# Kernel optimization log

Measured on AMD Instinct MI355X. Metric: run time of the kernel, lower is better.

Reference implementation:

```python
import jax, jax.numpy as jnp
import numpy as np
import math

NUM_HEADS = 8
RES_K = 9  # res_kernel_size


def setup_inputs() -> dict:
    key = jax.random.key(0)
    ks = jax.random.split(key, 6)
    N, C, h, w = 8, 256, 64, 64
    x = jax.random.normal(ks[0], (N, C, h, w), dtype=jnp.float32)
    w_qkv = jax.random.normal(ks[1], (3 * C, C), dtype=jnp.float32) * 0.02
    b_qkv = jax.random.normal(ks[2], (3 * C,), dtype=jnp.float32) * 0.02
    w_proj = jax.random.normal(ks[3], (C, C), dtype=jnp.float32) * 0.02
    b_proj = jax.random.normal(ks[4], (C,), dtype=jnp.float32) * 0.02
    w_dconv = jax.random.normal(ks[5], (NUM_HEADS, 1, RES_K, 1), dtype=jnp.float32) * 0.1
    return {"x": x, "w_qkv": w_qkv, "b_qkv": b_qkv,
            "w_proj": w_proj, "b_proj": b_proj, "w_dconv": w_dconv}


def _l2norm(t):
    # torch x / x.norm(dim=-1, keepdim=True): plain L2 norm, no eps
    return t / jnp.linalg.norm(t, axis=-1, keepdims=True)


def reference(x, w_qkv, b_qkv, w_proj, b_proj, w_dconv):
    N, C, h, w = x.shape
    H = NUM_HEADS
    D = C // H
    L = h * w
    xt = x.reshape(N, C, L).transpose(0, 2, 1)  # [N, L, C]
    qkv = xt @ w_qkv.T + b_qkv                   # [N, L, 3C]
    qkv = qkv.reshape(N, L, 3, H, D).transpose(2, 0, 3, 1, 4)  # [3, N, H, L, D]
    q, k, v = qkv[0], qkv[1], qkv[2]
    q = _l2norm(q)
    k = _l2norm(k)
    # depthwise conv over token dim: v as NCHW with C=H, H=L, W=D
    pad = RES_K // 2
    dconv_v = jax.lax.conv_general_dilated(
        v, w_dconv, window_strides=(1, 1), padding=[(pad, pad), (0, 0)],
        dimension_numbers=("NCHW", "OIHW", "NCHW"), feature_group_count=H)
    attn = jnp.einsum("nhld,nhle->nhde", k, v)   # [N, H, D, D]
    out = 0.5 * v + (1.0 / math.pi) * jnp.einsum("nhld,nhde->nhle", q, attn)
    out = _l2norm(out)
    out = out + dconv_v
    out = out.transpose(0, 2, 1, 3).reshape(N, L, C)  # [N, L, C]
    out = out @ w_proj.T + b_proj
    return out.transpose(0, 2, 1).reshape(N, C, h, w)
```

## Files before the change

### kernel.cpp

```cpp
#include <hip/hip_runtime.h>

#define NB 8
#define CC 256
#define HH 8
#define DD 32
#define LL 4096

typedef short v8s __attribute__((ext_vector_type(8)));
typedef float v4f __attribute__((ext_vector_type(4)));
typedef unsigned short v8u __attribute__((ext_vector_type(8)));
typedef unsigned short v4us __attribute__((ext_vector_type(4)));

__device__ __forceinline__ float4 ld4(const float* p) { return *(const float4*)p; }

__device__ __forceinline__ unsigned short f2bf(float f) {
    union { float f; unsigned int u; } v; v.f = f;
    unsigned int r = (v.u + 0x7FFFu + ((v.u >> 16) & 1u)) >> 16;
    return (unsigned short)r;
}
__device__ __forceinline__ float bf2f(unsigned short u) {
    union { unsigned int u; float f; } v; v.u = ((unsigned int)u) << 16;
    return v.f;
}

__device__ __forceinline__ void gl_lds16(const unsigned short* g, unsigned short* l) {
    __builtin_amdgcn_global_load_lds(
        (const __attribute__((address_space(1))) void*)g,
        (__attribute__((address_space(3))) void*)l, 16, 0, 0);
}

#define PADC 264
__global__ __launch_bounds__(256) void prep_k(
    const float* __restrict__ x, unsigned short* __restrict__ xb,
    const float* __restrict__ wq, const float* __restrict__ wp,
    unsigned short* __restrict__ dwq, unsigned short* __restrict__ dwp,
    float* __restrict__ attn)
{
    __shared__ unsigned short t[32][PADC];
    const int bid = blockIdx.x;
    if (bid < 1024) {
        const int n = bid >> 7;
        const int l0 = (bid & 127) * 32;
        const float* xn = x + (size_t)n * CC * LL;
        const int lam = threadIdx.x & 31;
        const int cb = threadIdx.x >> 5;
#pragma unroll
        for (int i = 0; i < 32; ++i) {
            int c = cb * 32 + i;
            t[lam][c] = f2bf(xn[(size_t)c * LL + l0 + lam]);
        }
        __syncthreads();
        unsigned short* dst = xb + ((size_t)n * LL + l0) * CC;
        const int tid = threadIdx.x;
#pragma unroll
        for (int i = 0; i < 4; ++i) {
            int f = i * 2048 + tid * 8;
            int lr = f >> 8;
            int c2 = f & 255;
            v8u val = *(const v8u*)&t[lr][c2];
            *(v8u*)(dst + f) = val;
        }
    } else {
        int ti = (bid - 1024) * 256 + threadIdx.x;
        if (ti < 24576) {
            int i = ti * 8;
            float4 f0 = ld4(wq + i), f1 = ld4(wq + i + 4);
            v8u o;
            o[0] = f2bf(f0.x); o[1] = f2bf(f0.y); o[2] = f2bf(f0.z); o[3] = f2bf(f0.w);
            o[4] = f2bf(f1.x); o[5] = f2bf(f1.y); o[6] = f2bf(f1.z); o[7] = f2bf(f1.w);
            *(v8u*)(dwq + i) = o;
        } else if (ti < 32768) {
            int i = (ti - 24576) * 8;
            float4 f0 = ld4(wp + i), f1 = ld4(wp + i + 4);
            v8u o;
            o[0] = f2bf(f0.x); o[1] = f2bf(f0.y); o[2] = f2bf(f0.z); o[3] = f2bf(f0.w);
            o[4] = f2bf(f1.x); o[5] = f2bf(f1.y); o[6] = f2bf(f1.z); o[7] = f2bf(f1.w);
            *(v8u*)(dwp + i) = o;
        } else {
            int i = (ti - 32768) * 4;
            *(float4*)(attn + i) = make_float4(0.f, 0.f, 0.f, 0.f);
        }
    }
}

__global__ __launch_bounds__(256, 2) void gemm_qkv_mfma(
    const unsigned short* __restrict__ xb, const unsigned short* __restrict__ wqb,
    const float* __restrict__ bqkv,
    unsigned short* __restrict__ q, unsigned short* __restrict__ k,
    unsigned short* __restrict__ v)
{
    __shared__ __align__(16) unsigned short xs[8192];
    __shared__ __align__(16) unsigned short wsb[16384];

    const int bid  = blockIdx.x;
    const int xcd  = bid & 7;
    const int slot = bid >> 3;
    const int jt   = slot % 3;
    const int p    = slot / 3;
    const int gp   = xcd * 32 + p;
    const int l0   = (gp & 31) * 128;
    const int n    = gp >> 5;
    const int j0   = jt * 256;

    const int tid = threadIdx.x;
    const int lane = tid & 63, wave = tid >> 6;
    const int wr = wave >> 1, wc = wave & 1;
    const int r = lane & 15, quad = lane >> 4;

    const int srow = wave * 8 + (lane >> 3);
    const int dchunk = (lane & 7) ^ (lane >> 3);
    const unsigned short* xg = xb + (size_t)n * LL * CC
                             + (size_t)(l0 + srow) * CC + dchunk * 8;
    const unsigned short* wg = wqb + (size_t)(j0 + srow) * CC + dchunk * 8;
    unsigned short* xls = xs + wave * 512 + lane * 8;
    unsigned short* wls = wsb + wave * 512 + lane * 8;

    v4f acc[8][4];
#pragma unroll
    for (int mi = 0; mi < 8; ++mi)
#pragma unroll
        for (int nj = 0; nj < 4; ++nj) acc[mi][nj] = (v4f)(0.f);

    const int jbase = wr * 128;
    const int lbase = wc * 64;

    for (int kt = 0; kt < 4; ++kt) {
        if (kt) __syncthreads();
        const int c0 = kt * 64;
#pragma unroll
        for (int i = 0; i < 4; ++i)
            gl_lds16(xg + (size_t)i * 32 * CC + c0, xls + i * 2048);
#pragma unroll
        for (int i = 0; i < 8; ++i)
            gl_lds16(wg + (size_t)i * 32 * CC + c0, wls + i * 2048);
        __syncthreads();

#pragma unroll
        for (int kk = 0; kk < 2; ++kk) {
            const int cfrag = kk * 4 + quad;
            const int s = cfrag ^ (r & 7);
            v8s b[4];
#pragma unroll
            for (int nj = 0; nj < 4; ++nj) {
                int lloc = lbase + nj * 16 + r;
                b[nj] = *(const v8s*)(xs + lloc * 64 + s * 8);
            }
            v8s a[8];
#pragma unroll
            for (int mi = 0; mi < 8; ++mi) {
                int jloc = jbase + mi * 16 + r;
                a[mi] = *(const v8s*)(wsb + jloc * 64 + s * 8);
            }
#pragma unroll
            for (int mi = 0; mi < 8; ++mi)
#pragma unroll
                for (int nj = 0; nj < 4; ++nj)
                    acc[mi][nj] = __builtin_amdgcn_mfma_f32_16x16x32_bf16(
                        a[mi], b[nj], acc[mi][nj], 0, 0, 0);
        }
    }

    unsigned short* base = (jt == 0 ? q : (jt == 1 ? k : v));

    float bias[8][4];
#pragma unroll
    for (int mi = 0; mi < 8; ++mi)
        *(float4*)bias[mi] = *(const float4*)(bqkv + j0 + jbase + mi * 16 + quad * 4);

    unsigned short* dstp[8];
#pragma unroll
    for (int mi = 0; mi < 8; ++mi) {
        int hh = wr * 4 + (mi >> 1);
        int d0 = (mi & 1) * 16 + quad * 4;
        dstp[mi] = base + (size_t)(n * HH + hh) * LL * DD + d0;
    }

    if (jt < 2) {
#pragma unroll
        for (int nj = 0; nj < 4; ++nj) {
            float t[8][4];
            float ss[4] = {0.f, 0.f, 0.f, 0.f};
#pragma unroll
            for (int mi = 0; mi < 8; ++mi)
#pragma unroll
                for (int reg = 0; reg < 4; ++reg) {
                    float val = acc[mi][nj][reg] + bias[mi][reg];
                    t[mi][reg] = val;
                    ss[mi >> 1] += val * val;
                }
#pragma unroll
            for (int h4 = 0; h4 < 4; ++h4) {
                ss[h4] += __shfl_xor(ss[h4], 16);
                ss[h4] += __shfl_xor(ss[h4], 32);
                ss[h4] = rsqrtf(ss[h4]);
            }
            size_t l = (size_t)(l0 + lbase + nj * 16 + r);
#pragma unroll
            for (int mi = 0; mi < 8; ++mi) {
                float rn = ss[mi >> 1];
                v4us pk;
#pragma unroll
                for (int reg = 0; reg < 4; ++reg) pk[reg] = f2bf(t[mi][reg] * rn);
                *(v4us*)(dstp[mi] + l * DD) = pk;
            }
        }
    } else {
#pragma unroll
        for (int nj = 0; nj < 4; ++nj) {
            size_t l = (size_t)(l0 + lbase + nj * 16 + r);
#pragma unroll
            for (int mi = 0; mi < 8; ++mi) {
                v4us pk;
#pragma unroll
                for (int reg = 0; reg < 4; ++reg)
                    pk[reg] = f2bf(acc[mi][nj][reg] + bias[mi][reg]);
                *(v4us*)(dstp[mi] + l * DD) = pk;
            }
        }
    }
}

__global__ __launch_bounds__(256) void attn_k(
    const unsigned short* __restrict__ k, const unsigned short* __restrict__ v,
    float* __restrict__ attn)
{
    __shared__ float red[4][1024];
    const int nh = blockIdx.y;
    const int wv = threadIdx.x >> 6;
    const int lane = threadIdx.x & 63;
    const int eg = lane & 7;
    const int dg = lane >> 3;
    const int l0 = blockIdx.x * 512 + wv * 128;
    const unsigned short* kb = k + (size_t)nh * LL * DD;
    const unsigned short* vb = v + (size_t)nh * LL * DD;
    float acc[4][4] = {};
#pragma unroll 4
    for (int l = l0; l < l0 + 128; ++l) {
        v4us k4 = *(const v4us*)(kb + (size_t)l * DD + dg * 4);
        v4us v4 = *(const v4us*)(vb + (size_t)l * DD + eg * 4);
        float ka[4] = {bf2f(k4[0]), bf2f(k4[1]), bf2f(k4[2]), bf2f(k4[3])};
        float va[4] = {bf2f(v4[0]), bf2f(v4[1]), bf2f(v4[2]), bf2f(v4[3])};
#pragma unroll
        for (int dp = 0; dp < 4; ++dp)
#pragma unroll
            for (int ep = 0; ep < 4; ++ep)
                acc[dp][ep] += ka[dp] * va[ep];
    }
#pragma unroll
    for (int dp = 0; dp < 4; ++dp)
#pragma unroll
        for (int ep = 0; ep < 4; ++ep)
            red[wv][(dg * 4 + dp) * 32 + eg * 4 + ep] = acc[dp][ep];
    __syncthreads();
    float* ap = attn + (size_t)nh * 1024;
    for (int i = threadIdx.x; i < 1024; i += 256)
        atomicAdd(&ap[i], red[0][i] + red[1][i] + red[2][i] + red[3][i]);
}

#define PTOK 64
#define VTP 40
__global__ __launch_bounds__(256, 2) void midproj_k(
    const unsigned short* __restrict__ q, const unsigned short* __restrict__ v,
    const float* __restrict__ attn, const float* __restrict__ wd,
    const unsigned short* __restrict__ wpb, const float* __restrict__ bp,
    float* __restrict__ out)
{
    __shared__ __align__(16) unsigned short vt[8 * 72 * VTP];
    __shared__ __align__(16) unsigned short smid[4 * 64 * 64];

    const int n  = blockIdx.y;
    const int l0 = blockIdx.x * PTOK;
    const int tid = threadIdx.x;
    const int lane = tid & 63, wave = tid >> 6;
    const int r = lane & 15, quad = lane >> 4;

    const unsigned short* vbase = v + (size_t)(n * HH) * LL * DD;
#pragma unroll
    for (int it = 0; it < 9; ++it) {
        int task = it * 256 + tid;
        int seg = task & 3;
        int hr = task >> 2;
        int row = hr % 72;
        int h = hr / 72;
        int l = l0 - 4 + row;
        v8u val;
        if (l >= 0 && l < LL)
            val = *(const v8u*)(vbase + ((size_t)h * LL + l) * DD + seg * 8);
        else
            val = (v8u)(unsigned short)0;
        *(v8u*)(&vt[hr * VTP + seg * 8]) = val;
    }
    __syncthreads();

    const float inv_pi = 0.31830988618379067f;
#pragma unroll
    for (int hi = 0; hi < 2; ++hi) {
        const int h = wave * 2 + hi;
        const int nh = n * HH + h;
        const unsigned short* qb = q + (size_t)nh * LL * DD;
        const unsigned short* vth = vt + h * 72 * VTP;

        v8s bfrag[2];
#pragma unroll
        for (int et = 0; et < 2; ++et) {
            int e = et * 16 + r;
#pragma unroll
            for (int j = 0; j < 8; ++j)
                ((unsigned short*)&bfrag[et])[j] =
                    f2bf(attn[(size_t)nh * 1024 + (quad * 8 + j) * 32 + e]);
        }
        float wc[9];
#pragma unroll
        for (int r9 = 0; r9 < 9; ++r9) wc[r9] = wd[h * 9 + r9];

#pragma unroll
        for (int lt = 0; lt < 4; ++lt) {
            const int tb = lt * 16;
            v8s afrag = *(const v8s*)(qb + (size_t)(l0 + tb + r) * DD + quad * 8);
            v4f acc[2] = {(v4f)(0.f), (v4f)(0.f)};
#pragma unroll
            for (int et = 0; et < 2; ++et)
                acc[et] = __builtin_amdgcn_mfma_f32_16x16x32_bf16(
                    afrag, bfrag[et], acc[et], 0, 0, 0);

            float vcol[2][12];
#pragma unroll
            for (int et = 0; et < 2; ++et) {
                int e = et * 16 + r;
#pragma unroll
                for (int o = 0; o < 12; ++o)
                    vcol[et][o] = bf2f(vth[(tb + quad * 4 + o) * VTP + e]);
            }

            float t[2][4], ss[4];
#pragma unroll
            for (int reg = 0; reg < 4; ++reg) {
                t[0][reg] = 0.5f * vcol[0][4 + reg] + inv_pi * acc[0][reg];
                t[1][reg] = 0.5f * vcol[1][4 + reg] + inv_pi * acc[1][reg];
                ss[reg] = t[0][reg] * t[0][reg] + t[1][reg] * t[1][reg];
            }
#pragma unroll
            for (int m = 1; m < 16; m <<= 1)
#pragma unroll
                for (int reg = 0; reg < 4; ++reg)
                    ss[reg] += __shfl_xor(ss[reg], m);
#pragma unroll
            for (int reg = 0; reg < 4; ++reg) ss[reg] = rsqrtf(ss[reg]);

#pragma unroll
            for (int et = 0; et < 2; ++et) {
                int c = h * 32 + et * 16 + r;
                int chunk = c >> 6, c6 = c & 63;
                int goff = c6 & 7;
#pragma unroll
                for (int reg = 0; reg < 4; ++reg) {
                    float dv = 0.f;
#pragma unroll
                    for (int r9 = 0; r9 < 9; ++r9) dv += wc[r9] * vcol[et][reg + r9];
                    int l = tb + quad * 4 + reg;
                    int g = (c6 >> 3) ^ (l & 7);
                    smid[chunk * 4096 + l * 64 + g * 8 + goff] =
                        f2bf(t[et][reg] * ss[reg] + dv);
                }
            }
        }
    }
    __syncthreads();

    const int jbase = wave * 64;
    v4f acc[4][4];
#pragma unroll
    for (int mi = 0; mi < 4; ++mi)
#pragma unroll
        for (int nj = 0; nj < 4; ++nj) acc[mi][nj] = (v4f)(0.f);

#pragma unroll
    for (int kt = 0; kt < 4; ++kt) {
        v8s a[4][2], b[4][2];
#pragma unroll
        for (int kk = 0; kk < 2; ++kk) {
            const int cfrag = kk * 4 + quad;
#pragma unroll
            for (int mi = 0; mi < 4; ++mi) {
                int j = jbase + mi * 16 + r;
                a[mi][kk] = *(const v8s*)(wpb + (size_t)j * CC + kt * 64 + cfrag * 8);
            }
            const int s = cfrag ^ (r & 7);
#pragma unroll
            for (int nj = 0; nj < 4; ++nj) {
                int lloc = nj * 16 + r;
                b[nj][kk] = *(const v8s*)(smid + kt * 4096 + lloc * 64 + s * 8);
            }
        }
#pragma unroll
        for (int kk = 0; kk < 2; ++kk)
#pragma unroll
            for (int mi = 0; mi < 4; ++mi)
#pragma unroll
                for (int nj = 0; nj < 4; ++nj)
                    acc[mi][nj] = __builtin_amdgcn_mfma_f32_16x16x32_bf16(
                        a[mi][kk], b[nj][kk], acc[mi][nj], 0, 0, 0);
    }

#pragma unroll
    for (int mi = 0; mi < 4; ++mi)
#pragma unroll
        for (int reg = 0; reg < 4; ++reg) {
            int j = jbase + mi * 16 + quad * 4 + reg;
            float bias = bp[j];
#pragma unroll
            for (int nj = 0; nj < 4; ++nj) {
                int l = l0 + nj * 16 + r;
                out[((size_t)n * CC + j) * LL + l] = acc[mi][nj][reg] + bias;
            }
        }
}

extern "C" void kernel_launch(void* const* d_in, const int* in_sizes, int n_in,
                              void* d_out, int out_size, void* d_ws, size_t ws_size,
                              hipStream_t stream)
{
    const float* x     = (const float*)d_in[0];
    const float* wqkv  = (const float*)d_in[1];
    const float* bqkv  = (const float*)d_in[2];
    const float* wproj = (const float*)d_in[3];
    const float* bproj = (const float*)d_in[4];
    const float* wd    = (const float*)d_in[5];
    float* out = (float*)d_out;

    const size_t QKV = (size_t)NB * HH * LL * DD;
    unsigned short* q = (unsigned short*)d_ws;
    unsigned short* k = q + QKV;
    unsigned short* v = k + QKV;
    float* attn = (float*)(v + QKV);
    unsigned short* xb = (unsigned short*)(attn + (size_t)NB * HH * DD * DD);
    unsigned short* wqb = xb + (size_t)NB * LL * CC;
    unsigned short* wpb = wqb + 3 * CC * CC;

    prep_k<<<1216, 256, 0, stream>>>(x, xb, wqkv, wproj, wqb, wpb, attn);
    gemm_qkv_mfma<<<768, 256, 0, stream>>>(xb, wqb, bqkv, q, k, v);
    attn_k<<<dim3(8, 64), 256, 0, stream>>>(k, v, attn);
    midproj_k<<<dim3(LL / PTOK, NB), 256, 0, stream>>>(q, v, attn, wd, wpb, bproj, out);
}
```

Measured before the change: 155.7 us.

## Fuse x transpose and bf16 conversion into QKV GEMM tile loads

Drops the separate prep pass that transposed x into a bf16 token-major buffer. The QKV GEMM now reads fp32 x directly with coalesced per-channel loads, converts to bf16 and writes into the swizzled LDS tile, and also zeroes the attn accumulator. This removes a full write and re-read of the bf16 activation copy (about 16 MB) plus most of a kernel launch. The cost is that each x tile is reread and reconverted by all three j-tiles, and the synchronous register-path loads replace async global-to-LDS copies, which may expose more latency.

New measurement: 158.9 us. 1.02x slower.

```diff
diff --git a/kernel.cpp b/kernel.cpp
--- a/kernel.cpp
+++ b/kernel.cpp
@@ -29,65 +29,33 @@
         (__attribute__((address_space(3))) void*)l, 16, 0, 0);
 }
 
-#define PADC 264
-__global__ __launch_bounds__(256) void prep_k(
-    const float* __restrict__ x, unsigned short* __restrict__ xb,
+__global__ __launch_bounds__(256) void prep_w(
     const float* __restrict__ wq, const float* __restrict__ wp,
-    unsigned short* __restrict__ dwq, unsigned short* __restrict__ dwp,
-    float* __restrict__ attn)
+    unsigned short* __restrict__ dwq, unsigned short* __restrict__ dwp)
 {
-    __shared__ unsigned short t[32][PADC];
-    const int bid = blockIdx.x;
-    if (bid < 1024) {
-        const int n = bid >> 7;
-        const int l0 = (bid & 127) * 32;
-        const float* xn = x + (size_t)n * CC * LL;
-        const int lam = threadIdx.x & 31;
-        const int cb = threadIdx.x >> 5;
-#pragma unroll
-        for (int i = 0; i < 32; ++i) {
-            int c = cb * 32 + i;
-            t[lam][c] = f2bf(xn[(size_t)c * LL + l0 + lam]);
-        }
-        __syncthreads();
-        unsigned short* dst = xb + ((size_t)n * LL + l0) * CC;
-        const int tid = threadIdx.x;
-#pragma unroll
-        for (int i = 0; i < 4; ++i) {
-            int f = i * 2048 + tid * 8;
-            int lr = f >> 8;
-            int c2 = f & 255;
-            v8u val = *(const v8u*)&t[lr][c2];
-            *(v8u*)(dst + f) = val;
-        }
+    int ti = blockIdx.x * 256 + threadIdx.x;
+    if (ti < 24576) {
+        int i = ti * 8;
+        float4 f0 = ld4(wq + i), f1 = ld4(wq + i + 4);
+        v8u o;
+        o[0] = f2bf(f0.x); o[1] = f2bf(f0.y); o[2] = f2bf(f0.z); o[3] = f2bf(f0.w);
+        o[4] = f2bf(f1.x); o[5] = f2bf(f1.y); o[6] = f2bf(f1.z); o[7] = f2bf(f1.w);
+        *(v8u*)(dwq + i) = o;
     } else {
-        int ti = (bid - 1024) * 256 + threadIdx.x;
-        if (ti < 24576) {
-            int i = ti * 8;
-            float4 f0 = ld4(wq + i), f1 = ld4(wq + i + 4);
-            v8u o;
-            o[0] = f2bf(f0.x); o[1] = f2bf(f0.y); o[2] = f2bf(f0.z); o[3] = f2bf(f0.w);
-            o[4] = f2bf(f1.x); o[5] = f2bf(f1.y); o[6] = f2bf(f1.z); o[7] = f2bf(f1.w);
-            *(v8u*)(dwq + i) = o;
-        } else if (ti < 32768) {
-            int i = (ti - 24576) * 8;
-            float4 f0 = ld4(wp + i), f1 = ld4(wp + i + 4);
-            v8u o;
-            o[0] = f2bf(f0.x); o[1] = f2bf(f0.y); o[2] = f2bf(f0.z); o[3] = f2bf(f0.w);
-            o[4] = f2bf(f1.x); o[5] = f2bf(f1.y); o[6] = f2bf(f1.z); o[7] = f2bf(f1.w);
-            *(v8u*)(dwp + i) = o;
-        } else {
-            int i = (ti - 32768) * 4;
-            *(float4*)(attn + i) = make_float4(0.f, 0.f, 0.f, 0.f);
-        }
+        int i = (ti - 24576) * 8;
+        float4 f0 = ld4(wp + i), f1 = ld4(wp + i + 4);
+        v8u o;
+        o[0] = f2bf(f0.x); o[1] = f2bf(f0.y); o[2] = f2bf(f0.z); o[3] = f2bf(f0.w);
+        o[4] = f2bf(f1.x); o[5] = f2bf(f1.y); o[6] = f2bf(f1.z); o[7] = f2bf(f1.w);
+        *(v8u*)(dwp + i) = o;
     }
 }
 
 __global__ __launch_bounds__(256, 2) void gemm_qkv_mfma(
-    const unsigned short* __restrict__ xb, const unsigned short* __restrict__ wqb,
+    const float* __restrict__ x, const unsigned short* __restrict__ wqb,
     const float* __restrict__ bqkv,
     unsigned short* __restrict__ q, unsigned short* __restrict__ k,
-    unsigned short* __restrict__ v)
+    unsigned short* __restrict__ v, float* __restrict__ attn)
 {
     __shared__ __align__(16) unsigned short xs[8192];
     __shared__ __align__(16) unsigned short wsb[16384];
@@ -107,13 +75,16 @@
     const int wr = wave >> 1, wc = wave & 1;
     const int r = lane & 15, quad = lane >> 4;
 
+    if (jt == 2) attn[gp * 256 + tid] = 0.f;
+
     const int srow = wave * 8 + (lane >> 3);
     const int dchunk = (lane & 7) ^ (lane >> 3);
-    const unsigned short* xg = xb + (size_t)n * LL * CC
-                             + (size_t)(l0 + srow) * CC + dchunk * 8;
     const unsigned short* wg = wqb + (size_t)(j0 + srow) * CC + dchunk * 8;
-    unsigned short* xls = xs + wave * 512 + lane * 8;
     unsigned short* wls = wsb + wave * 512 + lane * 8;
+
+    const int lw = tid & 127;
+    const int half = tid >> 7;
+    const float* xrow = x + (size_t)n * CC * LL + l0 + lw;
 
     v4f acc[8][4];
 #pragma unroll
@@ -128,11 +99,20 @@
         if (kt) __syncthreads();
         const int c0 = kt * 64;
 #pragma unroll
-        for (int i = 0; i < 4; ++i)
-            gl_lds16(xg + (size_t)i * 32 * CC + c0, xls + i * 2048);
-#pragma unroll
         for (int i = 0; i < 8; ++i)
             gl_lds16(wg + (size_t)i * 32 * CC + c0, wls + i * 2048);
+#pragma unroll
+        for (int chi = 0; chi < 4; ++chi) {
+            int ch = half * 4 + chi;
+            const float* src = xrow + (size_t)(c0 + ch * 8) * LL;
+            float f[8];
+#pragma unroll
+            for (int j = 0; j < 8; ++j) f[j] = src[(size_t)j * LL];
+            v8u o;
+#pragma unroll
+            for (int j = 0; j < 8; ++j) o[j] = f2bf(f[j]);
+            *(v8u*)(xs + lw * 64 + ((ch ^ (lw & 7)) * 8)) = o;
+        }
         __syncthreads();
 
 #pragma unroll
@@ -433,12 +413,11 @@
     unsigned short* k = q + QKV;
     unsigned short* v = k + QKV;
     float* attn = (float*)(v + QKV);
-    unsigned short* xb = (unsigned short*)(attn + (size_t)NB * HH * DD * DD);
-    unsigned short* wqb = xb + (size_t)NB * LL * CC;
+    unsigned short* wqb = (unsigned short*)(attn + (size_t)NB * HH * DD * DD);
     unsigned short* wpb = wqb + 3 * CC * CC;
 
-    prep_k<<<1216, 256, 0, stream>>>(x, xb, wqkv, wproj, wqb, wpb, attn);
-    gemm_qkv_mfma<<<768, 256, 0, stream>>>(xb, wqb, bqkv, q, k, v);
+    prep_w<<<128, 256, 0, stream>>>(wqkv, wproj, wqb, wpb);
+    gemm_qkv_mfma<<<768, 256, 0, stream>>>(x, wqb, bqkv, q, k, v, attn);
     attn_k<<<dim3(8, 64), 256, 0, stream>>>(k, v, attn);
     midproj_k<<<dim3(LL / PTOK, NB), 256, 0, stream>>>(q, v, attn, wd, wpb, bproj, out);
 }
```
